# Optimization experiments

Measured on AMD Instinct MI355X. Metric: run time of the kernel, lower is better.

The kernel has to match this reference:

```python
import jax, jax.numpy as jnp
import numpy as np

B = 2_000_000  # number of 6x6 stiffness matrices

def setup_inputs() -> dict:
    key = jax.random.key(0)
    C = jax.random.normal(key, (B, 6, 6), dtype=jnp.float32)
    return {"C": C}

def reference(C) -> jnp.ndarray:
    # matrix_power_4: C^4 via two repeated squarings, batched over leading dim
    C2 = jnp.matmul(C, C)   # [B,6,6]
    return jnp.matmul(C2, C2)
```

## Files before the change

kernel.cpp:

```cpp
#include <hip/hip_runtime.h>


#define WPB 64

#define GLOBAL_AS __attribute__((address_space(1)))
#define LDS_AS    __attribute__((address_space(3)))

typedef float f32x4 __attribute__((ext_vector_type(4)));

__device__ __forceinline__ void pow4_regs(float a[36])
{
    float b[36];
#pragma unroll
    for (int i = 0; i < 6; ++i)
#pragma unroll
        for (int j = 0; j < 6; ++j) {
            float s = a[i * 6 + 0] * a[0 * 6 + j];
#pragma unroll
            for (int k = 1; k < 6; ++k)
                s = fmaf(a[i * 6 + k], a[k * 6 + j], s);
            b[i * 6 + j] = s;
        }
#pragma unroll
    for (int i = 0; i < 6; ++i)
#pragma unroll
        for (int j = 0; j < 6; ++j) {
            float s = b[i * 6 + 0] * b[0 * 6 + j];
#pragma unroll
            for (int k = 1; k < 6; ++k)
                s = fmaf(b[i * 6 + k], b[k * 6 + j], s);
            a[i * 6 + j] = s;
        }
}

__global__ __launch_bounds__(WPB, 4) void matpow4_wave(
    const float* __restrict__ C, float* __restrict__ out, int nfull, int B)
{
    __shared__ f32x4 lds4[WPB * 9];

    const int lane = threadIdx.x;
    const int bid = blockIdx.x;

    if (bid < nfull) {
        const f32x4* __restrict__ src =
            reinterpret_cast<const f32x4*>(C) + (size_t)bid * (WPB * 9);
        f32x4* __restrict__ dst =
            reinterpret_cast<f32x4*>(out) + (size_t)bid * (WPB * 9);

#pragma unroll
        for (int k = 0; k < 9; ++k) {
            int f = k * WPB + lane;
            __builtin_amdgcn_global_load_lds(
                (const GLOBAL_AS void*)(src + f),
                (LDS_AS void*)(&lds4[f]), 16, 0, 0);
        }
        asm volatile("s_waitcnt vmcnt(0)" ::: "memory");
        __builtin_amdgcn_sched_barrier(0);

        float a[36];
#pragma unroll
        for (int j = 0; j < 9; ++j) {
            f32x4 v = lds4[lane * 9 + j];
            a[4 * j + 0] = v.x;
            a[4 * j + 1] = v.y;
            a[4 * j + 2] = v.z;
            a[4 * j + 3] = v.w;
        }
        pow4_regs(a);
#pragma unroll
        for (int j = 0; j < 9; ++j) {
            f32x4 v;
            v.x = a[4 * j + 0];
            v.y = a[4 * j + 1];
            v.z = a[4 * j + 2];
            v.w = a[4 * j + 3];
            lds4[lane * 9 + j] = v;
        }
        asm volatile("s_waitcnt lgkmcnt(0)" ::: "memory");
        __builtin_amdgcn_sched_barrier(0);

#pragma unroll
        for (int k = 0; k < 9; ++k) {
            int f = k * WPB + lane;
            dst[f] = lds4[f];
        }
    } else {
        int idx = nfull * WPB + lane;
        if (idx < B) {
            const f32x4* src = reinterpret_cast<const f32x4*>(C) + (size_t)idx * 9;
            float a[36];
#pragma unroll
            for (int j = 0; j < 9; ++j) {
                f32x4 v = src[j];
                a[4 * j + 0] = v.x;
                a[4 * j + 1] = v.y;
                a[4 * j + 2] = v.z;
                a[4 * j + 3] = v.w;
            }
            pow4_regs(a);
            f32x4* dst = reinterpret_cast<f32x4*>(out) + (size_t)idx * 9;
#pragma unroll
            for (int j = 0; j < 9; ++j) {
                f32x4 v;
                v.x = a[4 * j + 0];
                v.y = a[4 * j + 1];
                v.z = a[4 * j + 2];
                v.w = a[4 * j + 3];
                dst[j] = v;
            }
        }
    }
}

extern "C" void kernel_launch(void* const* d_in, const int* in_sizes, int n_in,
                              void* d_out, int out_size, void* d_ws, size_t ws_size,
                              hipStream_t stream)
{
    const float* C = (const float*)d_in[0];
    float* out = (float*)d_out;
    int B = in_sizes[0] / 36;

    int nfull = B / WPB;
    int grid = nfull + ((B % WPB) ? 1 : 0);
    matpow4_wave<<<grid, WPB, 0, stream>>>(C, out, nfull, B);
}
```

Baseline: 111.1 us.

## Process strips of chunks per wave with register prefetch and nontemporal access

Each 64-thread block now handles a strip of 8 chunks of 64 matrices instead of one. The next chunk's data is prefetched into registers while the current chunk is transposed through LDS and computed. Loads and stores use nontemporal hints, and the async global-to-LDS loads are replaced by register loads. The aim is to hide memory latency within each wave and to cut per-block launch overhead. The cost is fewer blocks, which means less parallelism and tail imbalance, plus more register pressure and a more complex tail-handling condition.

```diff
diff --git a/kernel.cpp b/kernel.cpp
--- a/kernel.cpp
+++ b/kernel.cpp
@@ -1,10 +1,8 @@
 #include <hip/hip_runtime.h>
 
 
-#define WPB 64
-
-#define GLOBAL_AS __attribute__((address_space(1)))
-#define LDS_AS    __attribute__((address_space(3)))
+#define WPB   64
+#define STRIP 8
 
 typedef float f32x4 __attribute__((ext_vector_type(4)));
 
@@ -33,61 +31,82 @@
         }
 }
 
-__global__ __launch_bounds__(WPB, 4) void matpow4_wave(
+__global__ __launch_bounds__(64, 3) void matpow4_wavepipe(
     const float* __restrict__ C, float* __restrict__ out, int nfull, int B)
 {
     __shared__ f32x4 lds4[WPB * 9];
 
     const int lane = threadIdx.x;
-    const int bid = blockIdx.x;
+    const long long c0 = (long long)blockIdx.x * STRIP;
 
-    if (bid < nfull) {
-        const f32x4* __restrict__ src =
-            reinterpret_cast<const f32x4*>(C) + (size_t)bid * (WPB * 9);
-        f32x4* __restrict__ dst =
-            reinterpret_cast<f32x4*>(out) + (size_t)bid * (WPB * 9);
+    const f32x4* __restrict__ srcAll = reinterpret_cast<const f32x4*>(C);
+    f32x4* __restrict__ dstAll = reinterpret_cast<f32x4*>(out);
 
+    if (c0 < nfull) {
+        const int nc = (int)min((long long)STRIP, (long long)nfull - c0);
+
+        f32x4 p[9];
+        {
+            const f32x4* src = srcAll + (size_t)c0 * (WPB * 9);
 #pragma unroll
-        for (int k = 0; k < 9; ++k) {
-            int f = k * WPB + lane;
-            __builtin_amdgcn_global_load_lds(
-                (const GLOBAL_AS void*)(src + f),
-                (LDS_AS void*)(&lds4[f]), 16, 0, 0);
+            for (int k = 0; k < 9; ++k)
+                p[k] = __builtin_nontemporal_load(src + k * WPB + lane);
         }
-        asm volatile("s_waitcnt vmcnt(0)" ::: "memory");
-        __builtin_amdgcn_sched_barrier(0);
 
-        float a[36];
+        for (int t = 0; t < nc; ++t) {
 #pragma unroll
-        for (int j = 0; j < 9; ++j) {
-            f32x4 v = lds4[lane * 9 + j];
-            a[4 * j + 0] = v.x;
-            a[4 * j + 1] = v.y;
-            a[4 * j + 2] = v.z;
-            a[4 * j + 3] = v.w;
+            for (int k = 0; k < 9; ++k)
+                lds4[k * WPB + lane] = p[k];
+
+            if (t + 1 < nc) {
+                const f32x4* src = srcAll + (size_t)(c0 + t + 1) * (WPB * 9);
+#pragma unroll
+                for (int k = 0; k < 9; ++k)
+                    p[k] = __builtin_nontemporal_load(src + k * WPB + lane);
+            }
+
+            asm volatile("s_waitcnt lgkmcnt(0)" ::: "memory");
+
+            {
+                float a[36];
+#pragma unroll
+                for (int j = 0; j < 9; ++j) {
+                    f32x4 v = lds4[lane * 9 + j];
+                    a[4 * j + 0] = v.x;
+                    a[4 * j + 1] = v.y;
+                    a[4 * j + 2] = v.z;
+                    a[4 * j + 3] = v.w;
+                }
+                pow4_regs(a);
+#pragma unroll
+                for (int j = 0; j < 9; ++j) {
+                    f32x4 v;
+                    v.x = a[4 * j + 0];
+                    v.y = a[4 * j + 1];
+                    v.z = a[4 * j + 2];
+                    v.w = a[4 * j + 3];
+                    lds4[lane * 9 + j] = v;
+                }
+            }
+            asm volatile("s_waitcnt lgkmcnt(0)" ::: "memory");
+
+            {
+                f32x4* dst = dstAll + (size_t)(c0 + t) * (WPB * 9);
+#pragma unroll
+                for (int k = 0; k < 9; ++k) {
+                    f32x4 v = lds4[k * WPB + lane];
+                    __builtin_nontemporal_store(v, dst + k * WPB + lane);
+                }
+            }
         }
-        pow4_regs(a);
-#pragma unroll
-        for (int j = 0; j < 9; ++j) {
-            f32x4 v;
-            v.x = a[4 * j + 0];
-            v.y = a[4 * j + 1];
-            v.z = a[4 * j + 2];
-            v.w = a[4 * j + 3];
-            lds4[lane * 9 + j] = v;
-        }
-        asm volatile("s_waitcnt lgkmcnt(0)" ::: "memory");
-        __builtin_amdgcn_sched_barrier(0);
+    }
 
-#pragma unroll
-        for (int k = 0; k < 9; ++k) {
-            int f = k * WPB + lane;
-            dst[f] = lds4[f];
-        }
-    } else {
-        int idx = nfull * WPB + lane;
-        if (idx < B) {
-            const f32x4* src = reinterpret_cast<const f32x4*>(C) + (size_t)idx * 9;
+    const long long tbase = (long long)nfull * WPB;
+    if (c0 >= nfull && (c0 - STRIP < nfull || blockIdx.x == gridDim.x - 1)) {
+        long long idx = tbase + lane;
+        if (idx < B && (c0 == ((nfull + STRIP - 1) / STRIP) * (long long)STRIP
+                        || blockIdx.x == gridDim.x - 1)) {
+            const f32x4* src = srcAll + (size_t)idx * 9;
             float a[36];
 #pragma unroll
             for (int j = 0; j < 9; ++j) {
@@ -98,7 +117,7 @@
                 a[4 * j + 3] = v.w;
             }
             pow4_regs(a);
-            f32x4* dst = reinterpret_cast<f32x4*>(out) + (size_t)idx * 9;
+            f32x4* dst = dstAll + (size_t)idx * 9;
 #pragma unroll
             for (int j = 0; j < 9; ++j) {
                 f32x4 v;
@@ -121,6 +140,7 @@
     int B = in_sizes[0] / 36;
 
     int nfull = B / WPB;
-    int grid = nfull + ((B % WPB) ? 1 : 0);
-    matpow4_wave<<<grid, WPB, 0, stream>>>(C, out, nfull, B);
+    int nstrip = (nfull + STRIP - 1) / STRIP;
+    int grid = nstrip + ((B % WPB) ? 1 : 0);
+    matpow4_wavepipe<<<grid, WPB, 0, stream>>>(C, out, nfull, B);
 }
```

Result: slower. 114.6 us (+3.1%).
